# Kernel optimization log

Hardware: AMD Instinct MI355X
Metric: run time of the kernel (lower is better)

The kernel has to match this reference:

```python
import jax, jax.numpy as jnp
import numpy as np

H = 16      # numHeads (== numKeyValueHeads since keyValueHeadsPerHead=1)
D = 128     # headDim


def setup_inputs() -> dict:
    key = jax.random.key(0)
    k1, k2, k3 = jax.random.split(key, 3)
    B, S, dim = 2, 2048, 2048
    x = jax.random.normal(k1, (B, S, dim), dtype=jnp.float32)
    # qkvProj: Linear(dim -> (H + 2*H)*D) without bias; torch Linear weight is [out, in]
    Wqkv = jax.random.normal(k2, ((H + 2 * H) * D, dim), dtype=jnp.float32) * 0.02
    # outProj: Linear(H*D -> dim) without bias
    Wout = jax.random.normal(k3, (dim, H * D), dtype=jnp.float32) * 0.02
    return {"x": x, "Wqkv": Wqkv, "Wout": Wout}


def reference(x, Wqkv, Wout):
    B, S, _ = x.shape
    qkv = jnp.einsum('bsd,ed->bse', x, Wqkv)           # [B, S, 3*H*D]
    qkv = qkv.reshape(B, S, 3 * H, D)
    q = qkv[:, :, :H]                                  # [B, S, H, D]
    k = qkv[:, :, H:2 * H]                             # [B, S, H, D]
    v = qkv[:, :, 2 * H:]                              # [B, S, H, D]
    # explicit QK^T / sqrt(d), softmax in fp32, then @ V (keyValueHeadsPerHead=1
    # collapses the group axis, leaving standard per-head attention)
    logits = jnp.einsum('bqhd,bkhd->bhqk', q, k) * (D ** -0.5)
    w = jax.nn.softmax(logits.astype(jnp.float32), axis=-1).astype(logits.dtype)
    out = jnp.einsum('bhqk,bkhd->bqhd', w, v).reshape(B, S, H * D)
    return jnp.einsum('bse,de->bsd', out, Wout)        # outProj
```

## Files before the change

kernel.cpp:

```cpp
#include <hip/hip_runtime.h>

typedef __bf16 bf16x8 __attribute__((ext_vector_type(8)));
typedef _Float16 f16;
typedef f16 f16x8 __attribute__((ext_vector_type(8)));
typedef float f32x4 __attribute__((ext_vector_type(4)));
typedef unsigned short u16;
typedef u16 u16x4 __attribute__((ext_vector_type(4)));

__device__ __forceinline__ u16 f2bf(float f) {
  unsigned u = __builtin_bit_cast(unsigned, f);
  u += 0x7FFFu + ((u >> 16) & 1u);
  return (u16)(u >> 16);
}

#define GLDS16(g, l) __builtin_amdgcn_global_load_lds(                     \
    (const __attribute__((address_space(1))) unsigned int*)(g),            \
    (__attribute__((address_space(3))) unsigned int*)(l), 16, 0, 0)

__device__ __forceinline__ f32x4 mfma16(bf16x8 a, bf16x8 b, f32x4 c) {
  return __builtin_amdgcn_mfma_f32_16x16x32_bf16(a, b, c, 0, 0, 0);
}
__device__ __forceinline__ f32x4 mfma16h(f16x8 a, f16x8 b, f32x4 c) {
  return __builtin_amdgcn_mfma_f32_16x16x32_f16(a, b, c, 0, 0, 0);
}

__global__ void cvt_bf16(const float* __restrict__ src, u16* __restrict__ dst,
                         int n4, int n4s, float scale) {
  int idx = blockIdx.x * blockDim.x + threadIdx.x;
  int stride = gridDim.x * blockDim.x;
  for (int i = idx; i < n4; i += stride) {
    float4 v = ((const float4*)src)[i];
    float sc = (i < n4s) ? scale : 1.0f;
    u16x4 o = { f2bf(v.x * sc), f2bf(v.y * sc), f2bf(v.z * sc), f2bf(v.w * sc) };
    ((u16x4*)dst)[i] = o;
  }
}

__global__ __launch_bounds__(256, 2) void gemm1_qkv(
    const u16* __restrict__ A, const u16* __restrict__ B,
    u16* __restrict__ QK, u16* __restrict__ VT) {
  __shared__ __align__(16) u16 LA[2][8192];
  __shared__ __align__(16) u16 LB[2][12288];
  constexpr int K = 2048;
  const int t = threadIdx.x, lane = t & 63, w = t >> 6;
  const int wm = w >> 1, wn = w & 1;
  const int l15 = lane & 15, lg = lane >> 4;
  const int l7 = l15 & 7;

  const int bid = blockIdx.x;
  const int wg = (bid & 7) * 128 + (bid >> 3);
  const int bx = wg & 31, by = wg >> 5;
  const int m0 = by * 128, n0 = bx * 192;

  const int srow = t >> 3;
  const int schunk = (t & 7) ^ (srow & 7);
  const u16* ga = A + (size_t)(m0 + srow) * K + schunk * 8;
  const u16* gb = B + (size_t)(n0 + srow) * K + schunk * 8;

  f32x4 acc[4][6] = {};

#define STG_A(ch, kt, bfi)                                                 \
    GLDS16(ga + (kt) * 64 + (size_t)(ch) * 32 * K, &LA[bfi][(ch) * 2048] + t * 8)
#define STG_B(ch, kt, bfi)                                                 \
    GLDS16(gb + (kt) * 64 + (size_t)(ch) * 32 * K, &LB[bfi][(ch) * 2048] + t * 8)

  STG_A(0, 0, 0); STG_A(2, 0, 0); STG_B(0, 0, 0);
  STG_B(1, 0, 0); STG_B(3, 0, 0); STG_B(4, 0, 0);
  STG_B(2, 0, 0); STG_B(5, 0, 0);
  STG_A(1, 0, 0); STG_A(3, 0, 0);
  asm volatile("s_waitcnt vmcnt(4)" ::: "memory");
  __builtin_amdgcn_s_barrier();

#pragma unroll 1
  for (int T = 0; T < 32; ++T) {
    const int p = T & 1, np = p ^ 1;
    const bool st = (T < 31);
    const u16* la = &LA[p][0];
    const u16* lb = &LB[p][0];
    bf16x8 aF[2][2], bLo[2][3], bHi[2][3];

#pragma unroll
    for (int kk = 0; kk < 2; ++kk) {
      const int cp = ((kk * 4 + lg) ^ l7) * 8;
#pragma unroll
      for (int i = 0; i < 2; ++i)
        aF[kk][i] = *(const bf16x8*)&la[(wm * 64 + i * 16 + l15) * 64 + cp];
#pragma unroll
      for (int j = 0; j < 3; ++j)
        bLo[kk][j] = *(const bf16x8*)&lb[(wn * 96 + j * 16 + l15) * 64 + cp];
    }
    if (st) {
      STG_A(0, T + 1, np); STG_A(2, T + 1, np); STG_B(0, T + 1, np);
      asm volatile("s_waitcnt vmcnt(5)" ::: "memory");
    } else {
      asm volatile("s_waitcnt vmcnt(2)" ::: "memory");
    }
    __builtin_amdgcn_s_barrier();
    asm volatile("s_waitcnt lgkmcnt(0)" ::: "memory");
    __builtin_amdgcn_sched_barrier(0);
    __builtin_amdgcn_s_setprio(1);
#pragma unroll
    for (int i = 0; i < 2; ++i)
#pragma unroll
      for (int j = 0; j < 3; ++j)
#pragma unroll
        for (int kk = 0; kk < 2; ++kk)
          acc[i][j] = mfma16(aF[kk][i], bLo[kk][j], acc[i][j]);
    __builtin_amdgcn_s_setprio(0);
    __builtin_amdgcn_s_barrier();

#pragma unroll
    for (int kk = 0; kk < 2; ++kk) {
      const int cp = ((kk * 4 + lg) ^ l7) * 8;
#pragma unroll
      for (int j = 0; j < 3; ++j)
        bHi[kk][j] = *(const bf16x8*)&lb[(wn * 96 + 48 + j * 16 + l15) * 64 + cp];
    }
    if (st) {
      STG_B(1, T + 1, np); STG_B(3, T + 1, np); STG_B(4, T + 1, np);
      asm volatile("s_waitcnt vmcnt(6)" ::: "memory");
    } else {
      asm volatile("s_waitcnt vmcnt(0)" ::: "memory");
    }
    __builtin_amdgcn_s_barrier();
    asm volatile("s_waitcnt lgkmcnt(0)" ::: "memory");
    __builtin_amdgcn_sched_barrier(0);
    __builtin_amdgcn_s_setprio(1);
#pragma unroll
    for (int i = 0; i < 2; ++i)
#pragma unroll
      for (int j = 0; j < 3; ++j)
#pragma unroll
        for (int kk = 0; kk < 2; ++kk)
          acc[i][3 + j] = mfma16(aF[kk][i], bHi[kk][j], acc[i][3 + j]);
    __builtin_amdgcn_s_setprio(0);
    __builtin_amdgcn_s_barrier();

#pragma unroll
    for (int kk = 0; kk < 2; ++kk) {
      const int cp = ((kk * 4 + lg) ^ l7) * 8;
#pragma unroll
      for (int i = 0; i < 2; ++i)
        aF[kk][i] = *(const bf16x8*)&la[(wm * 64 + 32 + i * 16 + l15) * 64 + cp];
    }
    if (st) { STG_B(2, T + 1, np); STG_B(5, T + 1, np); }
    __builtin_amdgcn_s_barrier();
    asm volatile("s_waitcnt lgkmcnt(0)" ::: "memory");
    __builtin_amdgcn_sched_barrier(0);
    __builtin_amdgcn_s_setprio(1);
#pragma unroll
    for (int i = 0; i < 2; ++i)
#pragma unroll
      for (int j = 0; j < 3; ++j)
#pragma unroll
        for (int kk = 0; kk < 2; ++kk)
          acc[2 + i][j] = mfma16(aF[kk][i], bLo[kk][j], acc[2 + i][j]);
    __builtin_amdgcn_s_setprio(0);
    __builtin_amdgcn_s_barrier();

    if (st) {
      STG_A(1, T + 1, np); STG_A(3, T + 1, np);
      asm volatile("s_waitcnt vmcnt(4)" ::: "memory");
    }
    __builtin_amdgcn_s_barrier();
    __builtin_amdgcn_s_setprio(1);
#pragma unroll
    for (int i = 0; i < 2; ++i)
#pragma unroll
      for (int j = 0; j < 3; ++j)
#pragma unroll
        for (int kk = 0; kk < 2; ++kk)
          acc[2 + i][3 + j] = mfma16(aF[kk][i], bHi[kk][j], acc[2 + i][3 + j]);
    __builtin_amdgcn_s_setprio(0);
    __builtin_amdgcn_s_barrier();
  }
#undef STG_A
#undef STG_B

  const int rb = m0 + wm * 64 + lg * 4;
  const int cb = n0 + wn * 96 + l15;
#pragma unroll
  for (int i = 0; i < 4; ++i) {
#pragma unroll
    for (int j = 0; j < 6; ++j) {
      const int row0 = rb + i * 16;
      const int col = cb + j * 16;
      if (col < 4096) {
#pragma unroll
        for (int jj = 0; jj < 4; ++jj)
          QK[(size_t)(row0 + jj) * 4096 + col] = f2bf(acc[i][j][jj]);
      } else {
        const int vcol = col - 4096;
        const int bb = row0 >> 11, s = row0 & 2047;
        auto h0 = __builtin_amdgcn_cvt_pkrtz(acc[i][j][0], acc[i][j][1]);
        auto h1 = __builtin_amdgcn_cvt_pkrtz(acc[i][j][2], acc[i][j][3]);
        uint2 pk;
        pk.x = __builtin_bit_cast(unsigned, h0);
        pk.y = __builtin_bit_cast(unsigned, h1);
        *(uint2*)&VT[((size_t)bb * 2048 + vcol) * 2048 + s] = pk;
      }
    }
  }
}

__global__ __launch_bounds__(256, 3) void gemm_bt(
    const u16* __restrict__ A, const u16* __restrict__ B,
    float* __restrict__ C, int M, int N, int K) {
  __shared__ __align__(16) u16 As[2][128 * 32];
  __shared__ __align__(16) u16 Bs[2][128 * 32];
  const int t = threadIdx.x;
  const int lane = t & 63;
  const int w = t >> 6;
  const int wm = w >> 1, wn = w & 1;
  const int l15 = lane & 15, lg = lane >> 4;
  const int m0 = blockIdx.y * 128, n0 = blockIdx.x * 128;
  f32x4 acc[4][4] = {};

  const int srow = t >> 2;
  const int schunk = (t & 3) ^ ((srow >> 1) & 3);
  const u16* ga = A + (size_t)(m0 + srow) * K + schunk * 8;
  const u16* gb = B + (size_t)(n0 + srow) * K + schunk * 8;
  const size_t half = (size_t)64 * K;
  const int ro = l15 * 32 + ((lg ^ ((l15 >> 1) & 3)) * 8);

#define STG(kt, bf) do {                                                   \
    const int ko_ = (kt) * 32;                                             \
    GLDS16(ga + ko_,        &As[bf][0] + t * 8);                           \
    GLDS16(ga + half + ko_, &As[bf][2048] + t * 8);                        \
    GLDS16(gb + ko_,        &Bs[bf][0] + t * 8);                           \
    GLDS16(gb + half + ko_, &Bs[bf][2048] + t * 8);                        \
  } while (0)

#define BODY(bf) do {                                                      \
    const u16* la_ = &As[bf][0];                                           \
    const u16* lb_ = &Bs[bf][0];                                           \
    bf16x8 af[4], bfr[4];                                                  \
    _Pragma("unroll")                                                      \
    for (int i_ = 0; i_ < 4; ++i_)                                         \
      af[i_] = *(const bf16x8*)&la_[(wm * 64 + i_ * 16) * 32 + ro];        \
    _Pragma("unroll")                                                      \
    for (int i_ = 0; i_ < 4; ++i_)                                         \
      bfr[i_] = *(const bf16x8*)&lb_[(wn * 64 + i_ * 16) * 32 + ro];       \
    __builtin_amdgcn_s_setprio(1);                                         \
    _Pragma("unroll")                                                      \
    for (int i_ = 0; i_ < 4; ++i_)                                         \
      _Pragma("unroll")                                                    \
      for (int j_ = 0; j_ < 4; ++j_)                                       \
        acc[i_][j_] = mfma16(af[i_], bfr[j_], acc[i_][j_]);                \
    __builtin_amdgcn_s_setprio(0);                                         \
  } while (0)

  const int NT = K / 32;
  STG(0, 0);
#pragma unroll 1
  for (int T = 0; T < NT - 1; ++T) {
    STG(T + 1, (T + 1) & 1);
    asm volatile("s_waitcnt vmcnt(4)" ::: "memory");
    __builtin_amdgcn_sched_barrier(0);
    __builtin_amdgcn_s_barrier();
    __builtin_amdgcn_sched_barrier(0);
    BODY(T & 1);
    asm volatile("s_waitcnt lgkmcnt(0)" ::: "memory");
    __builtin_amdgcn_sched_barrier(0);
    __builtin_amdgcn_s_barrier();
    __builtin_amdgcn_sched_barrier(0);
  }
  asm volatile("s_waitcnt vmcnt(0)" ::: "memory");
  __builtin_amdgcn_sched_barrier(0);
  __builtin_amdgcn_s_barrier();
  __builtin_amdgcn_sched_barrier(0);
  BODY((NT - 1) & 1);
#undef STG
#undef BODY

  const int rbase = m0 + wm * 64 + (lg << 2);
  const int cbase = n0 + wn * 64 + l15;
#pragma unroll
  for (int i = 0; i < 4; ++i)
#pragma unroll
    for (int j = 0; j < 4; ++j) {
      const int row0 = rbase + i * 16;
      const int col = cbase + j * 16;
#pragma unroll
      for (int jj = 0; jj < 4; ++jj)
        C[(size_t)(row0 + jj) * N + col] = acc[i][j][jj];
    }
}

#define PSTRIDE 72
__global__ __launch_bounds__(512, 1) void attn_fwd(
    const u16* __restrict__ qk, const u16* __restrict__ vt, u16* __restrict__ aout) {
  __shared__ __align__(16) u16 Ks[2][64 * 128];
  __shared__ __align__(16) u16 Vs[2][128 * 64];
  __shared__ __align__(16) u16 Pl[8][32 * PSTRIDE];
  const int t = threadIdx.x, lane = t & 63, w = t >> 6;
  const int bh = blockIdx.x;
  const int b = bh >> 4, h = bh & 15;
  const int q0 = blockIdx.y * 256 + w * 32;
  const int l15 = lane & 15, lg = lane >> 4;

  const u16* qp = qk + (size_t)b * 2048 * 4096 + h * 128;
  const u16* kp = qp + 2048;
  const u16* vtp = vt + (size_t)(b * 16 + h) * 128 * 2048;
  u16* op = aout + (size_t)b * 2048 * 2048 + h * 128;

  int ksoff[2], vsoff[2];
#pragma unroll
  for (int rd = 0; rd < 2; ++rd) {
    const int r = rd * 32 + (t >> 4);
    const int c = (t & 15) ^ (r & 15);
    ksoff[rd] = r * 4096 + c * 8;
    const int rv = rd * 64 + (t >> 3);
    const int cv = (t & 7) ^ (rv & 7);
    vsoff[rd] = rv * 2048 + cv * 8;
  }

  bf16x8 qf[2][4];
#pragma unroll
  for (int mi = 0; mi < 2; ++mi)
#pragma unroll
    for (int kd = 0; kd < 4; ++kd)
      qf[mi][kd] = *(const bf16x8*)&qp[(size_t)(q0 + mi * 16 + l15) * 4096 + kd * 32 + lg * 8];

  f32x4 o[2][8] = {};
  f32x4 lacc[2] = {};
  const f16x8 onesf = {f16(1.f), f16(1.f), f16(1.f), f16(1.f),
                       f16(1.f), f16(1.f), f16(1.f), f16(1.f)};
  u16* pw = &Pl[w][0];

#pragma unroll
  for (int rd = 0; rd < 2; ++rd) {
    GLDS16(kp + ksoff[rd], &Ks[0][0] + rd * 4096 + t * 8);
    GLDS16(vtp + vsoff[rd], &Vs[0][0] + rd * 4096 + t * 8);
  }
  __syncthreads();

  auto tile = [&](const u16* ksb, const u16* vsb, u16* kpre, u16* vpre, int nextit) {
    if (nextit < 32) {
      const size_t kt1 = (size_t)nextit * 64;
#pragma unroll
      for (int rd = 0; rd < 2; ++rd) {
        GLDS16(kp + kt1 * 4096 + ksoff[rd], kpre + rd * 4096 + t * 8);
        GLDS16(vtp + kt1 + vsoff[rd], vpre + rd * 4096 + t * 8);
      }
    }
    f32x4 sf[2][4];
    __builtin_amdgcn_s_setprio(1);
#pragma unroll
    for (int ni = 0; ni < 4; ++ni) {
      const int r = ni * 16 + l15;
      bf16x8 kf[4];
#pragma unroll
      for (int kd = 0; kd < 4; ++kd)
        kf[kd] = *(const bf16x8*)&ksb[r * 128 + (((kd * 4 + lg) ^ l15) * 8)];
#pragma unroll
      for (int mi = 0; mi < 2; ++mi) {
        f32x4 s = {0.f, 0.f, 0.f, 0.f};
        s = mfma16(kf[0], qf[mi][0], s);
        s = mfma16(kf[1], qf[mi][1], s);
        s = mfma16(kf[2], qf[mi][2], s);
        s = mfma16(kf[3], qf[mi][3], s);
        sf[mi][ni] = s;
      }
    }
    __builtin_amdgcn_s_setprio(0);

#pragma unroll
    for (int mi = 0; mi < 2; ++mi)
#pragma unroll
      for (int ni = 0; ni < 4; ++ni) {
        float p0 = exp2f(sf[mi][ni][0]);
        float p1 = exp2f(sf[mi][ni][1]);
        float p2 = exp2f(sf[mi][ni][2]);
        float p3 = exp2f(sf[mi][ni][3]);
        auto h0 = __builtin_amdgcn_cvt_pkrtz(p0, p1);
        auto h1 = __builtin_amdgcn_cvt_pkrtz(p2, p3);
        uint2 wv;
        wv.x = __builtin_bit_cast(unsigned, h0);
        wv.y = __builtin_bit_cast(unsigned, h1);
        *(uint2*)&pw[(mi * 16 + l15) * PSTRIDE + ni * 16 + lg * 4] = wv;
      }

    f16x8 pa[2][2];
#pragma unroll
    for (int mi = 0; mi < 2; ++mi)
#pragma unroll
      for (int ks = 0; ks < 2; ++ks)
        pa[mi][ks] = *(const f16x8*)&pw[(mi * 16 + l15) * PSTRIDE + ks * 32 + lg * 8];
    __builtin_amdgcn_s_setprio(1);
#pragma unroll
    for (int mi = 0; mi < 2; ++mi) {
      lacc[mi] = mfma16h(pa[mi][0], onesf, lacc[mi]);
      lacc[mi] = mfma16h(pa[mi][1], onesf, lacc[mi]);
    }
#pragma unroll
    for (int n2 = 0; n2 < 8; ++n2) {
      const int r = n2 * 16 + l15;
      f16x8 vf0 = *(const f16x8*)&vsb[r * 64 + (((0 * 4 + lg) ^ (l15 & 7)) * 8)];
      f16x8 vf1 = *(const f16x8*)&vsb[r * 64 + (((1 * 4 + lg) ^ (l15 & 7)) * 8)];
#pragma unroll
      for (int mi = 0; mi < 2; ++mi) {
        o[mi][n2] = mfma16h(pa[mi][0], vf0, o[mi][n2]);
        o[mi][n2] = mfma16h(pa[mi][1], vf1, o[mi][n2]);
      }
    }
    __builtin_amdgcn_s_setprio(0);
    __syncthreads();
  };

#pragma unroll 1
  for (int it = 0; it < 32; it += 2) {
    tile(&Ks[0][0], &Vs[0][0], &Ks[1][0], &Vs[1][0], it + 1);
    tile(&Ks[1][0], &Vs[1][0], &Ks[0][0], &Vs[0][0], it + 2);
  }

#pragma unroll
  for (int mi = 0; mi < 2; ++mi)
#pragma unroll
    for (int j = 0; j < 4; ++j) {
      float inv = 1.f / lacc[mi][j];
#pragma unroll
      for (int n2 = 0; n2 < 8; ++n2)
        op[(size_t)(q0 + mi * 16 + lg * 4 + j) * 2048 + n2 * 16 + l15] =
            f2bf(o[mi][n2][j] * inv);
    }
}

extern "C" void kernel_launch(void* const* d_in, const int* in_sizes, int n_in,
                              void* d_out, int out_size, void* d_ws, size_t ws_size,
                              hipStream_t stream) {
  const float* x    = (const float*)d_in[0];
  const float* Wqkv = (const float*)d_in[1];
  const float* Wout = (const float*)d_in[2];
  float* out = (float*)d_out;

  u16* ws = (u16*)d_ws;
  u16* xb    = ws;
  u16* wqkvb = ws + 8388608;
  u16* woutb = ws + 20971520;
  u16* qkbuf = ws + 25165824;
  u16* vtbuf = ws + 41943040;
  u16* aout  = xb;

  const float qscale = 0.08838834764831845f * 1.4426950408889634f;

  cvt_bf16<<<2048, 256, 0, stream>>>(x,    xb,    8388608 / 4, 0, 1.0f);
  cvt_bf16<<<2048, 256, 0, stream>>>(Wqkv, wqkvb, 12582912 / 4, 4194304 / 4, qscale);
  cvt_bf16<<<1024, 256, 0, stream>>>(Wout, woutb, 4194304 / 4, 0, 1.0f);

  gemm1_qkv<<<1024, 256, 0, stream>>>(xb, wqkvb, qkbuf, vtbuf);
  attn_fwd<<<dim3(32, 8, 1), 512, 0, stream>>>(qkbuf, vtbuf, aout);
  gemm_bt<<<dim3(16, 32), 256, 0, stream>>>(aout, woutb, out, 4096, 2048, 2048);
}
```

Baseline: 259.1 us.

## Rewrite output-projection GEMM with BK=64 quarter-staged pipeline and swizzled block order

Replaces the generic gemm_bt with a specialized gemm2_out that uses a K-tile of 64, an 8-way XOR LDS swizzle, and splits each iteration into four sub-phases. Global-to-LDS loads for the next tile are interleaved between MFMA quarters. Block IDs are also remapped so that blocks sharing a row panel are scheduled together, which improves L2 reuse. The aim is to hide load latency and cut loop overhead, at the cost of more barriers and lower occupancy (launch bounds drop from 3 to 2 blocks).

```diff
diff --git a/kernel.cpp b/kernel.cpp
--- a/kernel.cpp
+++ b/kernel.cpp
@@ -203,84 +203,153 @@
   }
 }
 
-__global__ __launch_bounds__(256, 3) void gemm_bt(
+__global__ __launch_bounds__(256, 2) void gemm2_out(
     const u16* __restrict__ A, const u16* __restrict__ B,
-    float* __restrict__ C, int M, int N, int K) {
-  __shared__ __align__(16) u16 As[2][128 * 32];
-  __shared__ __align__(16) u16 Bs[2][128 * 32];
-  const int t = threadIdx.x;
-  const int lane = t & 63;
-  const int w = t >> 6;
+    float* __restrict__ C) {
+  __shared__ __align__(16) u16 LA[2][8192];
+  __shared__ __align__(16) u16 LB[2][8192];
+  constexpr int K = 2048, N = 2048;
+  const int t = threadIdx.x, lane = t & 63, w = t >> 6;
   const int wm = w >> 1, wn = w & 1;
   const int l15 = lane & 15, lg = lane >> 4;
-  const int m0 = blockIdx.y * 128, n0 = blockIdx.x * 128;
-  f32x4 acc[4][4] = {};
-
-  const int srow = t >> 2;
-  const int schunk = (t & 3) ^ ((srow >> 1) & 3);
+  const int l7 = l15 & 7;
+
+  const int bid = blockIdx.x;
+  const int wg = (bid & 7) * 64 + (bid >> 3);
+  const int bx = wg & 15, by = wg >> 4;
+  const int m0 = by * 128, n0 = bx * 128;
+
+  const int srow = t >> 3;
+  const int schunk = (t & 7) ^ (srow & 7);
   const u16* ga = A + (size_t)(m0 + srow) * K + schunk * 8;
   const u16* gb = B + (size_t)(n0 + srow) * K + schunk * 8;
-  const size_t half = (size_t)64 * K;
-  const int ro = l15 * 32 + ((lg ^ ((l15 >> 1) & 3)) * 8);
-
-#define STG(kt, bf) do {                                                   \
-    const int ko_ = (kt) * 32;                                             \
-    GLDS16(ga + ko_,        &As[bf][0] + t * 8);                           \
-    GLDS16(ga + half + ko_, &As[bf][2048] + t * 8);                        \
-    GLDS16(gb + ko_,        &Bs[bf][0] + t * 8);                           \
-    GLDS16(gb + half + ko_, &Bs[bf][2048] + t * 8);                        \
-  } while (0)
-
-#define BODY(bf) do {                                                      \
-    const u16* la_ = &As[bf][0];                                           \
-    const u16* lb_ = &Bs[bf][0];                                           \
-    bf16x8 af[4], bfr[4];                                                  \
-    _Pragma("unroll")                                                      \
-    for (int i_ = 0; i_ < 4; ++i_)                                         \
-      af[i_] = *(const bf16x8*)&la_[(wm * 64 + i_ * 16) * 32 + ro];        \
-    _Pragma("unroll")                                                      \
-    for (int i_ = 0; i_ < 4; ++i_)                                         \
-      bfr[i_] = *(const bf16x8*)&lb_[(wn * 64 + i_ * 16) * 32 + ro];       \
-    __builtin_amdgcn_s_setprio(1);                                         \
-    _Pragma("unroll")                                                      \
-    for (int i_ = 0; i_ < 4; ++i_)                                         \
-      _Pragma("unroll")                                                    \
-      for (int j_ = 0; j_ < 4; ++j_)                                       \
-        acc[i_][j_] = mfma16(af[i_], bfr[j_], acc[i_][j_]);                \
-    __builtin_amdgcn_s_setprio(0);                                         \
-  } while (0)
-
-  const int NT = K / 32;
-  STG(0, 0);
+
+  f32x4 acc[4][4] = {};
+
+#define STG_A(ch, kt, bfi)                                                 \
+    GLDS16(ga + (kt) * 64 + (size_t)(ch) * 32 * K, &LA[bfi][(ch) * 2048] + t * 8)
+#define STG_B(ch, kt, bfi)                                                 \
+    GLDS16(gb + (kt) * 64 + (size_t)(ch) * 32 * K, &LB[bfi][(ch) * 2048] + t * 8)
+
+  STG_A(0, 0, 0); STG_A(2, 0, 0); STG_B(0, 0, 0); STG_B(2, 0, 0);
+  STG_B(1, 0, 0); STG_B(3, 0, 0);
+  STG_A(1, 0, 0); STG_A(3, 0, 0);
+  asm volatile("s_waitcnt vmcnt(4)" ::: "memory");
+  __builtin_amdgcn_s_barrier();
+
 #pragma unroll 1
-  for (int T = 0; T < NT - 1; ++T) {
-    STG(T + 1, (T + 1) & 1);
-    asm volatile("s_waitcnt vmcnt(4)" ::: "memory");
-    __builtin_amdgcn_sched_barrier(0);
-    __builtin_amdgcn_s_barrier();
-    __builtin_amdgcn_sched_barrier(0);
-    BODY(T & 1);
+  for (int T = 0; T < 32; ++T) {
+    const int p = T & 1, np = p ^ 1;
+    const bool st = (T < 31);
+    const u16* la = &LA[p][0];
+    const u16* lb = &LB[p][0];
+    bf16x8 aF[2][2], bLo[2][2], bHi[2][2];
+
+#pragma unroll
+    for (int kk = 0; kk < 2; ++kk) {
+      const int cp = ((kk * 4 + lg) ^ l7) * 8;
+#pragma unroll
+      for (int i = 0; i < 2; ++i) {
+        aF[kk][i]  = *(const bf16x8*)&la[(wm * 64 + i * 16 + l15) * 64 + cp];
+        bLo[kk][i] = *(const bf16x8*)&lb[(wn * 64 + i * 16 + l15) * 64 + cp];
+      }
+    }
+    if (st) {
+      STG_A(0, T + 1, np); STG_A(2, T + 1, np);
+      asm volatile("s_waitcnt vmcnt(4)" ::: "memory");
+    } else {
+      asm volatile("s_waitcnt vmcnt(2)" ::: "memory");
+    }
+    __builtin_amdgcn_s_barrier();
     asm volatile("s_waitcnt lgkmcnt(0)" ::: "memory");
     __builtin_amdgcn_sched_barrier(0);
-    __builtin_amdgcn_s_barrier();
+    __builtin_amdgcn_s_setprio(1);
+#pragma unroll
+    for (int i = 0; i < 2; ++i)
+#pragma unroll
+      for (int j = 0; j < 2; ++j)
+#pragma unroll
+        for (int kk = 0; kk < 2; ++kk)
+          acc[i][j] = mfma16(aF[kk][i], bLo[kk][j], acc[i][j]);
+    __builtin_amdgcn_s_setprio(0);
+    __builtin_amdgcn_s_barrier();
+
+#pragma unroll
+    for (int kk = 0; kk < 2; ++kk) {
+      const int cp = ((kk * 4 + lg) ^ l7) * 8;
+#pragma unroll
+      for (int j = 0; j < 2; ++j)
+        bHi[kk][j] = *(const bf16x8*)&lb[(wn * 64 + 32 + j * 16 + l15) * 64 + cp];
+    }
+    if (st) {
+      STG_B(0, T + 1, np); STG_B(2, T + 1, np);
+      asm volatile("s_waitcnt vmcnt(4)" ::: "memory");
+    } else {
+      asm volatile("s_waitcnt vmcnt(0)" ::: "memory");
+    }
+    __builtin_amdgcn_s_barrier();
+    asm volatile("s_waitcnt lgkmcnt(0)" ::: "memory");
     __builtin_amdgcn_sched_barrier(0);
-  }
-  asm volatile("s_waitcnt vmcnt(0)" ::: "memory");
-  __builtin_amdgcn_sched_barrier(0);
-  __builtin_amdgcn_s_barrier();
-  __builtin_amdgcn_sched_barrier(0);
-  BODY((NT - 1) & 1);
-#undef STG
-#undef BODY
-
-  const int rbase = m0 + wm * 64 + (lg << 2);
-  const int cbase = n0 + wn * 64 + l15;
+    __builtin_amdgcn_s_setprio(1);
+#pragma unroll
+    for (int i = 0; i < 2; ++i)
+#pragma unroll
+      for (int j = 0; j < 2; ++j)
+#pragma unroll
+        for (int kk = 0; kk < 2; ++kk)
+          acc[i][2 + j] = mfma16(aF[kk][i], bHi[kk][j], acc[i][2 + j]);
+    __builtin_amdgcn_s_setprio(0);
+    __builtin_amdgcn_s_barrier();
+
+#pragma unroll
+    for (int kk = 0; kk < 2; ++kk) {
+      const int cp = ((kk * 4 + lg) ^ l7) * 8;
+#pragma unroll
+      for (int i = 0; i < 2; ++i)
+        aF[kk][i] = *(const bf16x8*)&la[(wm * 64 + 32 + i * 16 + l15) * 64 + cp];
+    }
+    if (st) { STG_B(1, T + 1, np); STG_B(3, T + 1, np); }
+    __builtin_amdgcn_s_barrier();
+    asm volatile("s_waitcnt lgkmcnt(0)" ::: "memory");
+    __builtin_amdgcn_sched_barrier(0);
+    __builtin_amdgcn_s_setprio(1);
+#pragma unroll
+    for (int i = 0; i < 2; ++i)
+#pragma unroll
+      for (int j = 0; j < 2; ++j)
+#pragma unroll
+        for (int kk = 0; kk < 2; ++kk)
+          acc[2 + i][j] = mfma16(aF[kk][i], bLo[kk][j], acc[2 + i][j]);
+    __builtin_amdgcn_s_setprio(0);
+    __builtin_amdgcn_s_barrier();
+
+    if (st) {
+      STG_A(1, T + 1, np); STG_A(3, T + 1, np);
+      asm volatile("s_waitcnt vmcnt(4)" ::: "memory");
+    }
+    __builtin_amdgcn_s_barrier();
+    __builtin_amdgcn_s_setprio(1);
+#pragma unroll
+    for (int i = 0; i < 2; ++i)
+#pragma unroll
+      for (int j = 0; j < 2; ++j)
+#pragma unroll
+        for (int kk = 0; kk < 2; ++kk)
+          acc[2 + i][2 + j] = mfma16(aF[kk][i], bHi[kk][j], acc[2 + i][2 + j]);
+    __builtin_amdgcn_s_setprio(0);
+    __builtin_amdgcn_s_barrier();
+  }
+#undef STG_A
+#undef STG_B
+
+  const int rb = m0 + wm * 64 + lg * 4;
+  const int cb = n0 + wn * 64 + l15;
 #pragma unroll
   for (int i = 0; i < 4; ++i)
 #pragma unroll
     for (int j = 0; j < 4; ++j) {
-      const int row0 = rbase + i * 16;
-      const int col = cbase + j * 16;
+      const int row0 = rb + i * 16;
+      const int col = cb + j * 16;
 #pragma unroll
       for (int jj = 0; jj < 4; ++jj)
         C[(size_t)(row0 + jj) * N + col] = acc[i][j][jj];
@@ -450,5 +519,5 @@
 
   gemm1_qkv<<<1024, 256, 0, stream>>>(xb, wqkvb, qkbuf, vtbuf);
   attn_fwd<<<dim3(32, 8, 1), 512, 0, stream>>>(qkbuf, vtbuf, aout);
-  gemm_bt<<<dim3(16, 32), 256, 0, stream>>>(aout, woutb, out, 4096, 2048, 2048);
-}
+  gemm2_out<<<512, 256, 0, stream>>>(aout, woutb, out);
+}
```

Result: faster. 251.1 us (-3.1%).
